# Kernel optimization log

Measured on AMD Instinct MI355X. Metric: run time of the kernel, lower is better.

## Reference

```python
import jax, jax.numpy as jnp
import numpy as np

H = 512  # hidden_size; feature dim is 2H = 1024


def setup_inputs() -> dict:
    key = jax.random.key(0)
    ks = jax.random.split(key, 8)
    B, S, D2 = 32, 2048, 2 * H
    scale = 1.0 / np.sqrt(D2)
    return {
        "query": jax.random.normal(ks[0], (B, 4, H), dtype=jnp.float32),
        "keys": jax.random.normal(ks[1], (B, S, D2), dtype=jnp.float32),
        "Wa_w": jax.random.uniform(ks[2], (D2, D2), jnp.float32, -scale, scale),
        "Wa_b": jax.random.uniform(ks[3], (D2,), jnp.float32, -scale, scale),
        "Ua_w": jax.random.uniform(ks[4], (D2, D2), jnp.float32, -scale, scale),
        "Ua_b": jax.random.uniform(ks[5], (D2,), jnp.float32, -scale, scale),
        "Va_w": jax.random.uniform(ks[6], (1, D2), jnp.float32, -scale, scale),
        "Va_b": jax.random.uniform(ks[7], (1,), jnp.float32, -scale, scale),
    }


def reference(query, keys, Wa_w, Wa_b, Ua_w, Ua_b, Va_w, Va_b):
    B, D = query.shape[0], query.shape[-1]
    q = query.reshape(B, 2, -1, D)
    # last timestep of each direction, concatenated -> (B, 1, 2H)
    q = jnp.concatenate([q[:, 0, -1, :], q[:, 1, -1, :]], axis=-1)[:, None, :]
    # additive attention energies: (B, S, 2H)
    e = jnp.tanh((q @ Wa_w.T + Wa_b) + (keys @ Ua_w.T + Ua_b))
    scores = (e @ Va_w.T + Va_b)[..., 0][:, None, :]  # (B, 1, S)
    weights = jax.nn.softmax(scores, axis=-1)
    context = jnp.einsum("bqs,bsd->bqd", weights, keys)  # (B, 1, 2H)
    return context, weights
```

## Files before the change

### kernel.cpp

```cpp
#include <hip/hip_runtime.h>
#include <hip/hip_bf16.h>


typedef __attribute__((ext_vector_type(8))) short bf16x8;
typedef __attribute__((ext_vector_type(4))) float f32x4;

__device__ __forceinline__ unsigned pk_bf16(float x, float y) {
  union { __hip_bfloat162 h; unsigned u; } c;
  c.h = __float22bfloat162_rn(make_float2(x, y));
  return c.u;
}

__device__ __forceinline__ float fast_tanh(float x) {
  float e = __expf(2.0f * x);
  return 1.0f - 2.0f / (e + 1.0f);
}

typedef const __attribute__((address_space(1))) void* gas_t;
typedef __attribute__((address_space(3))) void* las_t;
__device__ __forceinline__ void ld_lds16(const void* g, void* l) {
  __builtin_amdgcn_global_load_lds((gas_t)g, (las_t)l, 16, 0, 0);
}

__global__ __launch_bounds__(256) void k_cvt(const float4* __restrict__ src,
                                             uint4* __restrict__ dst) {
  int i = blockIdx.x * 256 + threadIdx.x;
  float4 a = src[2 * i], b = src[2 * i + 1];
  uint4 o;
  o.x = pk_bf16(a.x, a.y);
  o.y = pk_bf16(a.z, a.w);
  o.z = pk_bf16(b.x, b.y);
  o.w = pk_bf16(b.z, b.w);
  dst[i] = o;
}

__global__ __launch_bounds__(256) void k_qw(const float* __restrict__ query,
                                            const float* __restrict__ Wa_w,
                                            const float* __restrict__ Wa_b,
                                            const float* __restrict__ Ua_b,
                                            float* __restrict__ qW) {
  const int jc = blockIdx.x, b = blockIdx.y, t = threadIdx.x;
  __shared__ float4 qloc[256];
  {
    const float* base = (t < 128) ? (query + b * 2048 + 512) : (query + b * 2048 + 1536 - 512);
    qloc[t] = *(const float4*)(base + t * 4);
  }
  __syncthreads();
  const int jl = t >> 3, ks = t & 7;
  const int j = jc * 32 + jl;
  const float* wrow = Wa_w + j * 1024;
  float s = 0.f;
  #pragma unroll
  for (int i = 0; i < 32; ++i) {
    float4 wv = *(const float4*)(wrow + i * 32 + ks * 4);
    float4 q4 = qloc[i * 8 + ks];
    s += wv.x * q4.x + wv.y * q4.y + wv.z * q4.z + wv.w * q4.w;
  }
  s += __shfl_xor(s, 1);
  s += __shfl_xor(s, 2);
  s += __shfl_xor(s, 4);
  if (ks == 0) qW[b * 1024 + j] = s + Wa_b[j] + Ua_b[j];
}

__global__ __launch_bounds__(256) void k_score2(const unsigned short* __restrict__ keys16,
                                                const unsigned short* __restrict__ Uab,
                                                const float* __restrict__ qW,
                                                const float* __restrict__ Va,
                                                float* __restrict__ scores) {
  __shared__ __align__(16) unsigned short As[128 * 64];
  __shared__ __align__(16) unsigned short Bs[128 * 64];
  const int jblk = blockIdx.x;
  const int rblk = blockIdx.y;
  const int t = threadIdx.x;
  const int lane = t & 63, w = t >> 6;
  const int wm = w >> 1, wn = w & 1;
  const int l15 = lane & 15, quad = lane >> 4;
  const int row0 = rblk * 128, j0 = jblk * 128;
  const int lr = lane >> 3;
  const int sg = (lane & 7) ^ lr;

  f32x4 acc[4][4];
  #pragma unroll
  for (int i = 0; i < 4; i++)
    #pragma unroll
    for (int j = 0; j < 4; j++) acc[i][j] = (f32x4){0.f, 0.f, 0.f, 0.f};

  const int rb = l15 & 7;
  const int aoff = (wm * 64 + l15) * 64;
  const int boff = (wn * 64 + l15) * 64;

  for (int k0 = 0; k0 < 1024; k0 += 64) {
    if (k0) __syncthreads();
    #pragma unroll
    for (int i = 0; i < 4; ++i) {
      const int c = w * 4 + i;
      const int row = c * 8 + lr;
      ld_lds16(keys16 + (size_t)(row0 + row) * 1024 + k0 + sg * 8, As + c * 512);
      ld_lds16(Uab + (size_t)(j0 + row) * 1024 + k0 + sg * 8, Bs + c * 512);
    }
    __syncthreads();
    #pragma unroll
    for (int ks = 0; ks < 2; ++ks) {
      const int x = ((ks * 4 + quad) ^ rb) * 8;
      bf16x8 af[4], bfr[4];
      #pragma unroll
      for (int i = 0; i < 4; i++) af[i] = *(const bf16x8*)(As + aoff + i * 1024 + x);
      #pragma unroll
      for (int i = 0; i < 4; i++) bfr[i] = *(const bf16x8*)(Bs + boff + i * 1024 + x);
      #pragma unroll
      for (int i = 0; i < 4; i++)
        #pragma unroll
        for (int j = 0; j < 4; j++)
          acc[i][j] = __builtin_amdgcn_mfma_f32_16x16x32_bf16(af[i], bfr[j], acc[i][j], 0, 0, 0);
    }
  }

  const int b = row0 >> 11;
  float va[4], qb[4];
  #pragma unroll
  for (int j = 0; j < 4; j++) {
    int jg = j0 + wn * 64 + j * 16 + l15;
    va[j] = Va[jg];
    qb[j] = qW[b * 1024 + jg];
  }
  #pragma unroll
  for (int i = 0; i < 4; i++) {
    #pragma unroll
    for (int r = 0; r < 4; r++) {
      float s = 0.f;
      #pragma unroll
      for (int j = 0; j < 4; j++)
        s += va[j] * fast_tanh(acc[i][j][r] + qb[j]);
      s += __shfl_xor(s, 1);
      s += __shfl_xor(s, 2);
      s += __shfl_xor(s, 4);
      s += __shfl_xor(s, 8);
      if (l15 == 0) {
        int rg = row0 + wm * 64 + i * 16 + quad * 4 + r;
        atomicAdd(&scores[rg], s);
      }
    }
  }
}

__global__ __launch_bounds__(256) void k_score1(const float* __restrict__ keys,
                                                const unsigned short* __restrict__ Uab,
                                                const float* __restrict__ qW,
                                                const float* __restrict__ Va,
                                                float* __restrict__ scores) {
  __shared__ __align__(16) unsigned short As[128 * 72];
  __shared__ __align__(16) unsigned short Bs[128 * 72];
  const int jblk = blockIdx.x, rblk = blockIdx.y;
  const int t = threadIdx.x;
  const int lane = t & 63, w = t >> 6;
  const int wm = w >> 1, wn = w & 1;
  const int l15 = lane & 15, quad = lane >> 4;
  const int row0 = rblk * 128, j0 = jblk * 128;
  f32x4 acc[4][4];
  #pragma unroll
  for (int i = 0; i < 4; i++)
    #pragma unroll
    for (int j = 0; j < 4; j++) acc[i][j] = (f32x4){0.f, 0.f, 0.f, 0.f};
  for (int k0 = 0; k0 < 1024; k0 += 64) {
    __syncthreads();
    #pragma unroll
    for (int i = 0; i < 8; ++i) {
      int c = i * 256 + t, m = c >> 4, f4 = c & 15;
      float4 v = *(const float4*)(keys + (size_t)(row0 + m) * 1024 + k0 + f4 * 4);
      uint2 p;
      p.x = pk_bf16(v.x, v.y);
      p.y = pk_bf16(v.z, v.w);
      *(uint2*)(As + m * 72 + f4 * 4) = p;
    }
    #pragma unroll
    for (int i = 0; i < 4; ++i) {
      int c = i * 256 + t, j = c >> 3, k8 = c & 7;
      *(uint4*)(Bs + j * 72 + k8 * 8) = *(const uint4*)(Uab + (size_t)(j0 + j) * 1024 + k0 + k8 * 8);
    }
    __syncthreads();
    #pragma unroll
    for (int ks = 0; ks < 2; ++ks) {
      bf16x8 af[4], bfr[4];
      #pragma unroll
      for (int i = 0; i < 4; i++)
        af[i] = *(const bf16x8*)(As + (wm * 64 + i * 16 + l15) * 72 + ks * 32 + quad * 8);
      #pragma unroll
      for (int i = 0; i < 4; i++)
        bfr[i] = *(const bf16x8*)(Bs + (wn * 64 + i * 16 + l15) * 72 + ks * 32 + quad * 8);
      #pragma unroll
      for (int i = 0; i < 4; i++)
        #pragma unroll
        for (int j = 0; j < 4; j++)
          acc[i][j] = __builtin_amdgcn_mfma_f32_16x16x32_bf16(af[i], bfr[j], acc[i][j], 0, 0, 0);
    }
  }
  const int b = row0 >> 11;
  float va[4], qb[4];
  #pragma unroll
  for (int j = 0; j < 4; j++) {
    int jg = j0 + wn * 64 + j * 16 + l15;
    va[j] = Va[jg];
    qb[j] = qW[b * 1024 + jg];
  }
  #pragma unroll
  for (int i = 0; i < 4; i++)
    #pragma unroll
    for (int r = 0; r < 4; r++) {
      float s = 0.f;
      #pragma unroll
      for (int j = 0; j < 4; j++) s += va[j] * fast_tanh(acc[i][j][r] + qb[j]);
      s += __shfl_xor(s, 1);
      s += __shfl_xor(s, 2);
      s += __shfl_xor(s, 4);
      s += __shfl_xor(s, 8);
      if (l15 == 0) atomicAdd(&scores[row0 + wm * 64 + i * 16 + quad * 4 + r], s);
    }
}

__global__ __launch_bounds__(256) void k_softmax(const float* __restrict__ scores,
                                                 float* __restrict__ wout) {
  const int b = blockIdx.x, t = threadIdx.x;
  const int lane = t & 63, w = t >> 6;
  __shared__ float red[4];
  float v[8];
  float mx = -1e30f;
  #pragma unroll
  for (int i = 0; i < 8; i++) {
    v[i] = scores[b * 2048 + i * 256 + t];
    mx = fmaxf(mx, v[i]);
  }
  #pragma unroll
  for (int off = 1; off < 64; off <<= 1) mx = fmaxf(mx, __shfl_xor(mx, off));
  if (lane == 0) red[w] = mx;
  __syncthreads();
  mx = fmaxf(fmaxf(red[0], red[1]), fmaxf(red[2], red[3]));
  float sum = 0.f;
  #pragma unroll
  for (int i = 0; i < 8; i++) {
    v[i] = __expf(v[i] - mx);
    sum += v[i];
  }
  #pragma unroll
  for (int off = 1; off < 64; off <<= 1) sum += __shfl_xor(sum, off);
  __syncthreads();
  if (lane == 0) red[w] = sum;
  __syncthreads();
  sum = red[0] + red[1] + red[2] + red[3];
  float inv = 1.0f / sum;
  #pragma unroll
  for (int i = 0; i < 8; i++) wout[b * 2048 + i * 256 + t] = v[i] * inv;
}

__global__ __launch_bounds__(256) void k_context(const float* __restrict__ keys,
                                                 const float* __restrict__ wts,
                                                 float* __restrict__ ctx) {
  const int sc = blockIdx.x;
  const int b  = blockIdx.y;
  const int t  = threadIdx.x;
  __shared__ float wl[64];
  if (t < 64) wl[t] = wts[b * 2048 + sc * 64 + t];
  __syncthreads();
  const float4* kp = (const float4*)(keys + ((size_t)(b * 2048 + sc * 64) << 10)) + t;
  float4 a = {0.f, 0.f, 0.f, 0.f};
  #pragma unroll 8
  for (int s = 0; s < 64; ++s) {
    float4 kv = kp[s * 256];
    float wv = wl[s];
    a.x += wv * kv.x; a.y += wv * kv.y; a.z += wv * kv.z; a.w += wv * kv.w;
  }
  float* o = ctx + b * 1024 + t * 4;
  atomicAdd(o + 0, a.x);
  atomicAdd(o + 1, a.y);
  atomicAdd(o + 2, a.z);
  atomicAdd(o + 3, a.w);
}

extern "C" void kernel_launch(void* const* d_in, const int* in_sizes, int n_in,
                              void* d_out, int out_size, void* d_ws, size_t ws_size,
                              hipStream_t stream) {
  const float* query = (const float*)d_in[0];
  const float* keys  = (const float*)d_in[1];
  const float* Wa_w  = (const float*)d_in[2];
  const float* Wa_b  = (const float*)d_in[3];
  const float* Ua_w  = (const float*)d_in[4];
  const float* Ua_b  = (const float*)d_in[5];
  const float* Va_w  = (const float*)d_in[6];

  float* scores = (float*)d_ws;
  float* qW     = scores + 65536;
  unsigned short* Uab    = (unsigned short*)(qW + 32768);
  unsigned short* keys16 = Uab + 1024 * 1024;
  const size_t NEED_A = 2490368ull + 134217728ull;

  float* ctx = (float*)d_out;
  float* wts = ctx + 32768;

  hipMemsetAsync(scores, 0, 65536 * sizeof(float), stream);
  hipMemsetAsync(ctx, 0, 32768 * sizeof(float), stream);

  k_cvt<<<512, 256, 0, stream>>>((const float4*)Ua_w, (uint4*)Uab);
  k_qw<<<dim3(32, 32), 256, 0, stream>>>(query, Wa_w, Wa_b, Ua_b, qW);

  if (ws_size >= NEED_A) {
    k_cvt<<<32768, 256, 0, stream>>>((const float4*)keys, (uint4*)keys16);
    k_score2<<<dim3(8, 512), 256, 0, stream>>>(keys16, Uab, qW, Va_w, scores);
  } else {
    k_score1<<<dim3(8, 512), 256, 0, stream>>>(keys, Uab, qW, Va_w, scores);
  }

  k_softmax<<<32, 256, 0, stream>>>(scores, wts);
  k_context<<<dim3(32, 32), 256, 0, stream>>>(keys, wts, ctx);
}
```

Measured before the change: 622.5 us.

## Merge conversion kernels, swizzle score grid, fold ctx memset into softmax

Merges the two fp32-to-bf16 conversion launches into one kernel covering both Ua_w and keys, with each thread now handling one float4 instead of two. Removes the ctx memset by zeroing ctx inside the softmax kernel. Remaps the score GEMM grid to a 1D launch grouped so that 8 row blocks share adjacent column blocks for better L2 reuse, and hoists global address computation out of the k-loop. This trims launch overhead and improves cache locality, but the narrower per-thread conversion work may lower bandwidth efficiency.

```diff
diff --git a/kernel.cpp b/kernel.cpp
--- a/kernel.cpp
+++ b/kernel.cpp
@@ -22,16 +22,21 @@
   __builtin_amdgcn_global_load_lds((gas_t)g, (las_t)l, 16, 0, 0);
 }
 
-__global__ __launch_bounds__(256) void k_cvt(const float4* __restrict__ src,
-                                             uint4* __restrict__ dst) {
-  int i = blockIdx.x * 256 + threadIdx.x;
-  float4 a = src[2 * i], b = src[2 * i + 1];
-  uint4 o;
-  o.x = pk_bf16(a.x, a.y);
-  o.y = pk_bf16(a.z, a.w);
-  o.z = pk_bf16(b.x, b.y);
-  o.w = pk_bf16(b.z, b.w);
-  dst[i] = o;
+__global__ __launch_bounds__(256) void k_cvt_all(const float4* __restrict__ keys,
+                                                 const float4* __restrict__ ua,
+                                                 uint2* __restrict__ keys16,
+                                                 uint2* __restrict__ ua16) {
+  size_t i = (size_t)blockIdx.x * 256 + threadIdx.x;
+  const float4* src;
+  uint2* dst;
+  size_t idx;
+  if (i < 262144) { src = ua; dst = ua16; idx = i; }
+  else            { src = keys; dst = keys16; idx = i - 262144; }
+  float4 v = src[idx];
+  uint2 o;
+  o.x = pk_bf16(v.x, v.y);
+  o.y = pk_bf16(v.z, v.w);
+  dst[idx] = o;
 }
 
 __global__ __launch_bounds__(256) void k_qw(const float* __restrict__ query,
@@ -69,8 +74,10 @@
                                                 float* __restrict__ scores) {
   __shared__ __align__(16) unsigned short As[128 * 64];
   __shared__ __align__(16) unsigned short Bs[128 * 64];
-  const int jblk = blockIdx.x;
-  const int rblk = blockIdx.y;
+  const int h = blockIdx.x;
+  const int x = h & 7, g = h >> 3;
+  const int jblk = g & 7;
+  const int rblk = x + ((g >> 3) << 3);
   const int t = threadIdx.x;
   const int lane = t & 63, w = t >> 6;
   const int wm = w >> 1, wn = w & 1;
@@ -89,24 +96,26 @@
   const int aoff = (wm * 64 + l15) * 64;
   const int boff = (wn * 64 + l15) * 64;
 
+  const unsigned short* ga = keys16 + (size_t)(row0 + (w * 4) * 8 + lr) * 1024 + sg * 8;
+  const unsigned short* gb = Uab + (size_t)(j0 + (w * 4) * 8 + lr) * 1024 + sg * 8;
+
   for (int k0 = 0; k0 < 1024; k0 += 64) {
     if (k0) __syncthreads();
     #pragma unroll
     for (int i = 0; i < 4; ++i) {
       const int c = w * 4 + i;
-      const int row = c * 8 + lr;
-      ld_lds16(keys16 + (size_t)(row0 + row) * 1024 + k0 + sg * 8, As + c * 512);
-      ld_lds16(Uab + (size_t)(j0 + row) * 1024 + k0 + sg * 8, Bs + c * 512);
+      ld_lds16(ga + (size_t)i * 8 * 1024 + k0, As + c * 512);
+      ld_lds16(gb + (size_t)i * 8 * 1024 + k0, Bs + c * 512);
     }
     __syncthreads();
     #pragma unroll
     for (int ks = 0; ks < 2; ++ks) {
-      const int x = ((ks * 4 + quad) ^ rb) * 8;
+      const int xf = ((ks * 4 + quad) ^ rb) * 8;
       bf16x8 af[4], bfr[4];
       #pragma unroll
-      for (int i = 0; i < 4; i++) af[i] = *(const bf16x8*)(As + aoff + i * 1024 + x);
-      #pragma unroll
-      for (int i = 0; i < 4; i++) bfr[i] = *(const bf16x8*)(Bs + boff + i * 1024 + x);
+      for (int i = 0; i < 4; i++) af[i] = *(const bf16x8*)(As + aoff + i * 1024 + xf);
+      #pragma unroll
+      for (int i = 0; i < 4; i++) bfr[i] = *(const bf16x8*)(Bs + boff + i * 1024 + xf);
       #pragma unroll
       for (int i = 0; i < 4; i++)
         #pragma unroll
@@ -218,9 +227,11 @@
 }
 
 __global__ __launch_bounds__(256) void k_softmax(const float* __restrict__ scores,
-                                                 float* __restrict__ wout) {
+                                                 float* __restrict__ wout,
+                                                 float* __restrict__ ctx) {
   const int b = blockIdx.x, t = threadIdx.x;
   const int lane = t & 63, w = t >> 6;
+  *(float4*)(ctx + b * 1024 + t * 4) = (float4){0.f, 0.f, 0.f, 0.f};
   __shared__ float red[4];
   float v[8];
   float mx = -1e30f;
@@ -296,18 +307,18 @@
   float* wts = ctx + 32768;
 
   hipMemsetAsync(scores, 0, 65536 * sizeof(float), stream);
-  hipMemsetAsync(ctx, 0, 32768 * sizeof(float), stream);
-
-  k_cvt<<<512, 256, 0, stream>>>((const float4*)Ua_w, (uint4*)Uab);
   k_qw<<<dim3(32, 32), 256, 0, stream>>>(query, Wa_w, Wa_b, Ua_b, qW);
 
   if (ws_size >= NEED_A) {
-    k_cvt<<<32768, 256, 0, stream>>>((const float4*)keys, (uint4*)keys16);
-    k_score2<<<dim3(8, 512), 256, 0, stream>>>(keys16, Uab, qW, Va_w, scores);
+    k_cvt_all<<<66560, 256, 0, stream>>>((const float4*)keys, (const float4*)Ua_w,
+                                         (uint2*)keys16, (uint2*)Uab);
+    k_score2<<<4096, 256, 0, stream>>>(keys16, Uab, qW, Va_w, scores);
   } else {
+    k_cvt_all<<<1024, 256, 0, stream>>>((const float4*)keys, (const float4*)Ua_w,
+                                        (uint2*)keys16, (uint2*)Uab);
     k_score1<<<dim3(8, 512), 256, 0, stream>>>(keys, Uab, qW, Va_w, scores);
   }
 
-  k_softmax<<<32, 256, 0, stream>>>(scores, wts);
+  k_softmax<<<32, 256, 0, stream>>>(scores, wts, ctx);
   k_context<<<dim3(32, 32), 256, 0, stream>>>(keys, wts, ctx);
 }
```

New measurement: 591.9 us. 1.05x faster.
